# Performance work log

Measured on AMD Instinct MI355X. Metric: run time of the kernel, lower is better.

The kernel has to match this reference:

```python
import jax, jax.numpy as jnp
import numpy as np

DIM = 1024
NUM_HEADS = 16
HEAD_DIM = DIM // NUM_HEADS  # 64; only used for the softmax scale


def setup_inputs() -> dict:
    key = jax.random.key(0)
    ks = jax.random.split(key, 9)
    s = 1.0 / np.sqrt(DIM)
    return {
        "x": jax.random.normal(ks[0], (2, 4096, DIM), dtype=jnp.float32),
        "Wq": jax.random.normal(ks[1], (DIM, DIM), dtype=jnp.float32) * s,
        "bq": jnp.zeros((DIM,), dtype=jnp.float32),
        "Wk": jax.random.normal(ks[2], (DIM, DIM), dtype=jnp.float32) * s,
        "bk": jnp.zeros((DIM,), dtype=jnp.float32),
        "Wv": jax.random.normal(ks[3], (DIM, DIM), dtype=jnp.float32) * s,
        "bv": jnp.zeros((DIM,), dtype=jnp.float32),
        "Wo": jax.random.normal(ks[4], (DIM, DIM), dtype=jnp.float32) * s,
        "bo": jnp.zeros((DIM,), dtype=jnp.float32),
    }


def reference(x, Wq, bq, Wk, bk, Wv, bv, Wo, bo):
    # Projections (nn.Linear equivalents)
    q = jnp.einsum("bsd,df->bsf", x, Wq) + bq
    k = jnp.einsum("bsd,df->bsf", x, Wk) + bk
    v = jnp.einsum("bsd,df->bsf", x, Wv) + bv
    # Full-dim attention (no head split); scale uses head_dim per original code.
    scale = 1.0 / np.sqrt(HEAD_DIM)
    scores = jnp.einsum("bqd,bkd->bqk", q, k) * scale  # [B, S, S]
    attn = jax.nn.softmax(scores, axis=-1)
    out = jnp.einsum("bqk,bkd->bqd", attn, v)
    return jnp.einsum("bsd,df->bsf", out, Wo) + bo
```

## Files before the change

### kernel.cpp

```cpp
#include <hip/hip_runtime.h>

typedef unsigned short u16;
using bf16x8  = __attribute__((ext_vector_type(8))) __bf16;
using floatx4 = __attribute__((ext_vector_type(4))) float;

__device__ __forceinline__ u16 f2bf(float f) {
  unsigned int u = __builtin_bit_cast(unsigned int, f);
  u += 0x7fffu + ((u >> 16) & 1u);
  return (u16)(u >> 16);
}
__device__ __forceinline__ float bf2f(u16 h) {
  unsigned int u = ((unsigned int)h) << 16;
  return __builtin_bit_cast(float, u);
}

#define AS1(p) ((const __attribute__((address_space(1))) void*)(p))
#define AS3(p) ((__attribute__((address_space(3))) void*)(p))

#define GEMM_PROLOGUE_AT(bmv, bnv)                                           \
  __shared__ u16 As[128 * 32];                                               \
  __shared__ u16 Bs[128 * 32];                                               \
  const int tid  = threadIdx.x;                                              \
  const int wave = tid >> 6, lane = tid & 63;                                \
  const int wm = (wave >> 1) * 64, wn = (wave & 1) * 64;                     \
  const long bm = (bmv), bn = (bnv);                                         \
  floatx4 acc[4][4] = {};                                                    \
  const int srow = lane >> 2;                                                \
  const int scol = (lane & 3) * 8;                                           \
  const int c0 = wave * 2, c1 = c0 + 1;                                      \
  const int fr = lane & 15;                                                  \
  const int kq = (lane >> 4) * 8;                                            \
  const int oc = (lane >> 4) * 4;

#define GEMM_PROLOGUE() GEMM_PROLOGUE_AT((long)blockIdx.y * 128, (long)blockIdx.x * 128)

#define GEMM_STAGE(Ab, Bb, K, k0)                                            \
    __syncthreads();                                                         \
    __builtin_amdgcn_global_load_lds(AS1(Ab + (long)(c0*16 + srow)*K + k0 + scol), AS3(As + c0*512), 16, 0, 0); \
    __builtin_amdgcn_global_load_lds(AS1(Ab + (long)(c1*16 + srow)*K + k0 + scol), AS3(As + c1*512), 16, 0, 0); \
    __builtin_amdgcn_global_load_lds(AS1(Bb + (long)(c0*16 + srow)*K + k0 + scol), AS3(Bs + c0*512), 16, 0, 0); \
    __builtin_amdgcn_global_load_lds(AS1(Bb + (long)(c1*16 + srow)*K + k0 + scol), AS3(Bs + c1*512), 16, 0, 0); \
    __syncthreads();                                                         \
    bf16x8 af[4], bfv[4];                                                    \
    _Pragma("unroll")                                                        \
    for (int mi = 0; mi < 4; ++mi)                                           \
      af[mi] = *(const bf16x8*)(As + (wm + mi*16 + fr)*32 + kq);             \
    _Pragma("unroll")                                                        \
    for (int ni = 0; ni < 4; ++ni)                                           \
      bfv[ni] = *(const bf16x8*)(Bs + (wn + ni*16 + fr)*32 + kq);

#define GEMM_KSTEP_SWAP(Ab, Bb, K, k0)                                       \
  {                                                                          \
    GEMM_STAGE(Ab, Bb, K, k0)                                                \
    _Pragma("unroll")                                                        \
    for (int mi = 0; mi < 4; ++mi)                                           \
      _Pragma("unroll")                                                      \
      for (int ni = 0; ni < 4; ++ni)                                         \
        acc[mi][ni] = __builtin_amdgcn_mfma_f32_16x16x32_bf16(bfv[ni], af[mi], acc[mi][ni], 0, 0, 0); \
  }

#define NE_PROLOGUE(bmv, bnv)                                                \
  __shared__ u16 lds[65536];                                    \
  const int tid = threadIdx.x;                                               \
  const int w = tid >> 6, lane = tid & 63;                                   \
  const int wm = (w >> 2) * 128, wn = (w & 3) * 64;                          \
  const int wm16 = (w >> 2) * 8;           \
  const int wn4  = (w & 3) * 4;            \
  const long bm = (bmv), bn = (bnv);                                         \
  floatx4 acc[8][4] = {};                                                    \
  const int fr = lane & 15;                                                  \
  const int kq = (lane >> 4) * 8;                                            \
  const int oc = (lane >> 4) * 4;                                            \
         \
  const int swz  = (lane * 16) ^ (((lane >> 5) & 1) << 5);                   \
  const int srow = swz >> 6;                  \
  const int scol = (swz & 63) >> 1;           \
  const int st0  = w * 2;                      \
                        \
  const int aoff = fr * 64 + ((kq * 2) ^ (((fr >> 3) & 1) << 5));

#define NE_SETUP_PTRS(Abp, Bbp, ldK)                                         \
  const u16* A0p = (Abp) + (long)(st0 * 16 + srow) * (ldK) + scol;           \
  const u16* A1p = A0p + 16L * (ldK);                                        \
  const u16* B0p = (Bbp) + (long)(st0 * 16 + srow) * (ldK) + scol;           \
  const u16* B1p = B0p + 16L * (ldK);

#define NE_SA(T)                                                             \
  { u16* d_ = lds + (((T) & 3) * 16384) + st0 * 512;                         \
    long o_ = (long)(T) * 32;                                                \
    __builtin_amdgcn_global_load_lds(AS1(A0p + o_), AS3(d_), 16, 0, 0);      \
    __builtin_amdgcn_global_load_lds(AS1(A1p + o_), AS3(d_ + 512), 16, 0, 0); }
#define NE_SB(T)                                                             \
  { u16* d_ = lds + (((T) & 3) * 16384) + 8192 + st0 * 512;                  \
    long o_ = (long)(T) * 32;                                                \
    __builtin_amdgcn_global_load_lds(AS1(B0p + o_), AS3(d_), 16, 0, 0);      \
    __builtin_amdgcn_global_load_lds(AS1(B1p + o_), AS3(d_ + 512), 16, 0, 0); }

#define NE_TILE_G(T, NT, MF)                                                 \
  {                                                                          \
    const char* sb_ = (const char*)lds + ((T) & 3) * 32768;                  \
    if ((T) + 2 < (NT)) NE_SB((T) + 2)                                       \
    if ((T) + 3 < (NT)) NE_SA((T) + 3)                                       \
    bf16x8 af[4], bf[4];                                                     \
    _Pragma("unroll")                                                        \
    for (int i = 0; i < 4; ++i)                                              \
      af[i] = *(const bf16x8*)(sb_ + (wm16 + i) * 1024 + aoff);              \
    _Pragma("unroll")                                                        \
    for (int i = 0; i < 4; ++i)                                              \
      bf[i] = *(const bf16x8*)(sb_ + 16384 + (wn4 + i) * 1024 + aoff);       \
    asm volatile("s_waitcnt lgkmcnt(0)" ::: "memory");                       \
    __builtin_amdgcn_sched_barrier(0);                                       \
    __builtin_amdgcn_s_setprio(1);                                           \
    _Pragma("unroll")                                                        \
    for (int mi = 0; mi < 4; ++mi)                                           \
      _Pragma("unroll")                                                      \
      for (int ni = 0; ni < 4; ++ni)                                         \
        acc[mi][ni] = MF(mi, ni, acc[mi][ni]);                               \
    __builtin_amdgcn_s_setprio(0);                                           \
    _Pragma("unroll")                                                        \
    for (int i = 0; i < 4; ++i)                                              \
      af[i] = *(const bf16x8*)(sb_ + (wm16 + 4 + i) * 1024 + aoff);          \
    asm volatile("s_waitcnt lgkmcnt(0)" ::: "memory");                       \
    __builtin_amdgcn_sched_barrier(0);                                       \
    __builtin_amdgcn_s_setprio(1);                                           \
    _Pragma("unroll")                                                        \
    for (int mi = 0; mi < 4; ++mi)                                           \
      _Pragma("unroll")                                                      \
      for (int ni = 0; ni < 4; ++ni)                                         \
        acc[4 + mi][ni] = MF(mi, ni, acc[4 + mi][ni]);                       \
    __builtin_amdgcn_s_setprio(0);                                           \
    if ((T) < (NT) - 3)       { asm volatile("s_waitcnt vmcnt(6)" ::: "memory"); } \
    else if ((T) == (NT) - 3) { asm volatile("s_waitcnt vmcnt(4)" ::: "memory"); } \
    else if ((T) == (NT) - 2) { asm volatile("s_waitcnt vmcnt(0)" ::: "memory"); } \
    __builtin_amdgcn_s_barrier();                                            \
    __builtin_amdgcn_sched_barrier(0);                                       \
  }

#define NE_MF_SWAP(mi, ni, c) __builtin_amdgcn_mfma_f32_16x16x32_bf16(bf[ni], af[mi], (c), 0, 0, 0)
#define NE_MF_NS(mi, ni, c)   __builtin_amdgcn_mfma_f32_16x16x32_bf16(af[mi], bf[ni], (c), 0, 0, 0)
#define NE_TILE(T, NT)    NE_TILE_G(T, NT, NE_MF_SWAP)
#define NE_TILE_NS(T, NT) NE_TILE_G(T, NT, NE_MF_NS)

#define NE_START()                                                           \
  NE_SA(0) NE_SB(0) NE_SA(1) NE_SB(1) NE_SA(2)                               \
  asm volatile("s_waitcnt vmcnt(6)" ::: "memory");                           \
  __builtin_amdgcn_s_barrier();                                              \
  __builtin_amdgcn_sched_barrier(0);

__global__ __launch_bounds__(256) void gemm_bt(
    const u16* __restrict__ A, const u16* __restrict__ Bt,
    float* __restrict__ Cout, const float* __restrict__ bias, int N, int K)
{
  GEMM_PROLOGUE();
  const u16* Ab = A + bm * K;
  const u16* Bb = Bt + bn * K;
  for (int k0 = 0; k0 < K; k0 += 32) GEMM_KSTEP_SWAP(Ab, Bb, K, k0);

#pragma unroll
  for (int mi = 0; mi < 4; ++mi) {
    long row = bm + wm + mi*16 + fr;
#pragma unroll
    for (int ni = 0; ni < 4; ++ni) {
      long colb = bn + wn + ni*16 + oc;
      float4 bv4 = *(const float4*)(bias + colb);
      float4 o;
      o.x = acc[mi][ni][0] + bv4.x;
      o.y = acc[mi][ni][1] + bv4.y;
      o.z = acc[mi][ni][2] + bv4.z;
      o.w = acc[mi][ni][3] + bv4.w;
      *(float4*)(Cout + row * N + colb) = o;
    }
  }
}

__global__ __launch_bounds__(512, 2) void gemm_qk_exp(
    const u16* __restrict__ q, const u16* __restrict__ k,
    u16* __restrict__ probs, float* __restrict__ lpartT, float alpha)
{
  const int N = 4096;
  const int xcd = blockIdx.x;
  const int j = blockIdx.y;
  const long b = xcd >> 2;
  const int by = (xcd & 3) * 4 + (j & 3);
  const int bx = j >> 2;

  NE_PROLOGUE((long)by * 256, (long)bx * 256);
  const u16* Ab = q + b * 4096 * 1024 + bm * 1024;
  const u16* Bb = k + b * 4096 * 1024 + bn * 1024;
  NE_SETUP_PTRS(Ab, Bb, 1024);
  u16* P = probs + b * 4096L * 4096;
  float* lp = lpartT + b * 4096 * 64;

  NE_START()
  for (int T = 0; T < 32; ++T) NE_TILE(T, 32)

  const float a2 = alpha * 1.44269504f;
  const int cg = bx * 4 + (w & 3);
#pragma unroll
  for (int mi = 0; mi < 8; ++mi) {
    long row = bm + wm + mi * 16 + fr;
    float rs = 0.f;
#pragma unroll
    for (int ni = 0; ni < 4; ++ni) {
      long colb = bn + wn + ni * 16 + oc;
      float e0 = __builtin_amdgcn_exp2f(acc[mi][ni][0] * a2);
      float e1 = __builtin_amdgcn_exp2f(acc[mi][ni][1] * a2);
      float e2 = __builtin_amdgcn_exp2f(acc[mi][ni][2] * a2);
      float e3 = __builtin_amdgcn_exp2f(acc[mi][ni][3] * a2);
      rs += (e0 + e1) + (e2 + e3);
      ushort4 o;
      o.x = f2bf(e0); o.y = f2bf(e1); o.z = f2bf(e2); o.w = f2bf(e3);
      *(ushort4*)(P + row * N + colb) = o;
    }
    rs += __shfl_xor(rs, 16);
    rs += __shfl_xor(rs, 32);
    if (lane < 16)
      lp[(bm + wm + mi * 16 + lane) * 64 + cg] = rs;
  }
}

__global__ __launch_bounds__(512, 2) void gemm_pv_splitk2(
    const u16* __restrict__ probs, const u16* __restrict__ vT,
    u16* __restrict__ pA, u16* __restrict__ pB)
{
  const int xcd = blockIdx.x;
  const int j = blockIdx.y;
  const long b = xcd >> 2;
  const int sp = (xcd >> 1) & 1;
  const int by = (xcd & 1) * 8 + (j & 7);
  const int bx = j >> 3;

  NE_PROLOGUE((long)by * 256, (long)bx * 256);
  const u16* Ab = probs + b * 4096L * 4096 + bm * 4096 + sp * 2048;
  const u16* Bb = vT + b * 1024L * 4096 + bn * 4096 + sp * 2048;
  NE_SETUP_PTRS(Ab, Bb, 4096);
  u16* part = (b ? pB : pA) + (long)sp * 4096 * 1024;

  NE_START()
  for (int T = 0; T < 64; ++T) NE_TILE(T, 64)

#pragma unroll
  for (int mi = 0; mi < 8; ++mi) {
    long row = bm + wm + mi * 16 + fr;
#pragma unroll
    for (int ni = 0; ni < 4; ++ni) {
      long colb = bn + wn + ni * 16 + oc;
      ushort4 o;
      o.x = f2bf(acc[mi][ni][0]);
      o.y = f2bf(acc[mi][ni][1]);
      o.z = f2bf(acc[mi][ni][2]);
      o.w = f2bf(acc[mi][ni][3]);
      *(ushort4*)(part + row * 1024 + colb) = o;
    }
  }
}

__global__ __launch_bounds__(512, 2) void gemm_qkv(
    const u16* __restrict__ A, const u16* __restrict__ Bt,
    u16* __restrict__ qb, u16* __restrict__ kb, u16* __restrict__ vT,
    const float* __restrict__ bq, const float* __restrict__ bk,
    const float* __restrict__ bv)
{
  const int xcd = blockIdx.x;
  const int j = blockIdx.y;
  const int by = xcd * 4 + (j & 3);
  const int bx = j >> 2;

  NE_PROLOGUE((long)by * 256, (long)bx * 256);
  const u16* Ab = A + bm * 1024;
  const u16* Bb = Bt + bn * 1024;
  NE_SETUP_PTRS(Ab, Bb, 1024);

  if (bn < 2048) {
    NE_START()
    for (int T = 0; T < 32; ++T) NE_TILE(T, 32)
    u16* C = (bn < 1024) ? qb : kb;
    const float* bias = (bn < 1024) ? bq : bk;
#pragma unroll
    for (int mi = 0; mi < 8; ++mi) {
      long row = bm + wm + mi * 16 + fr;
#pragma unroll
      for (int ni = 0; ni < 4; ++ni) {
        long colg = bn + wn + ni * 16 + oc;
        long cc = colg & 1023;
        float4 bv4 = *(const float4*)(bias + cc);
        ushort4 o;
        o.x = f2bf(acc[mi][ni][0] + bv4.x);
        o.y = f2bf(acc[mi][ni][1] + bv4.y);
        o.z = f2bf(acc[mi][ni][2] + bv4.z);
        o.w = f2bf(acc[mi][ni][3] + bv4.w);
        *(ushort4*)(C + row * 1024 + cc) = o;
      }
    }
  } else {
    NE_START()
    for (int T = 0; T < 32; ++T) NE_TILE_NS(T, 32)
    const int orow = (lane >> 4) * 4;
    const long b_ = bm >> 12;
    const long s0 = (bm & 4095) + wm;
    u16* vb = vT + b_ * (1024L * 4096);
#pragma unroll
    for (int ni = 0; ni < 4; ++ni) {
      long d = bn + wn + ni * 16 + fr - 2048;
      float bvv = bv[d];
#pragma unroll
      for (int mi = 0; mi < 8; ++mi) {
        long s = s0 + mi * 16 + orow;
        ushort4 o;
        o.x = f2bf(acc[mi][ni][0] + bvv);
        o.y = f2bf(acc[mi][ni][1] + bvv);
        o.z = f2bf(acc[mi][ni][2] + bvv);
        o.w = f2bf(acc[mi][ni][3] + bvv);
        *(ushort4*)(vb + d * 4096L + s) = o;
      }
    }
  }
}

__global__ __launch_bounds__(256) void reduce2_div_row(
    const u16* __restrict__ pA, const u16* __restrict__ pB,
    const float* __restrict__ lpartT, u16* __restrict__ ob)
{
  const int row = blockIdx.x;
  const long b = blockIdx.y;
  const int tid = threadIdx.x;
  const u16* part = b ? pB : pA;
  const float* lp = lpartT + b * 4096 * 64;
  __shared__ float sl;
  if (tid < 64) {
    float s = lp[(long)row * 64 + tid];
#pragma unroll
    for (int off = 32; off; off >>= 1) s += __shfl_down(s, off);
    if (tid == 0) sl = s;
  }
  __syncthreads();
  const float inv = 1.0f / sl;
  const long base = (long)row * 1024 + tid * 4;
  float acc4[4] = {0.f, 0.f, 0.f, 0.f};
#pragma unroll
  for (int s = 0; s < 2; ++s) {
    ushort4 p = *(const ushort4*)(part + (long)s * 4096 * 1024 + base);
    acc4[0] += bf2f(p.x); acc4[1] += bf2f(p.y);
    acc4[2] += bf2f(p.z); acc4[3] += bf2f(p.w);
  }
  ushort4 o;
  o.x = f2bf(acc4[0] * inv);
  o.y = f2bf(acc4[1] * inv);
  o.z = f2bf(acc4[2] * inv);
  o.w = f2bf(acc4[3] * inv);
  *(ushort4*)(ob + b * 4096L * 1024 + base) = o;
}

__global__ __launch_bounds__(256) void prep(
    const float* __restrict__ x, u16* __restrict__ xb,
    const float* __restrict__ W0, const float* __restrict__ W1,
    const float* __restrict__ W2, const float* __restrict__ W3,
    u16* __restrict__ O0, u16* __restrict__ O1,
    u16* __restrict__ O2, u16* __restrict__ O3)
{
  __shared__ float tile[32][33];
  int blk = blockIdx.x;
  if (blk < 8192) {
    int i = blk * 256 + threadIdx.x;
    float4 f = ((const float4*)x)[i];
    ushort4 o;
    o.x = f2bf(f.x); o.y = f2bf(f.y); o.z = f2bf(f.z); o.w = f2bf(f.w);
    ((ushort4*)xb)[i] = o;
  } else {
    blk -= 8192;
    const int z = blk >> 10, t = blk & 1023;
    const float* in = (z == 0) ? W0 : (z == 1) ? W1 : (z == 2) ? W2 : W3;
    u16* outp = (z == 0) ? O0 : (z == 1) ? O1 : (z == 2) ? O2 : O3;
    const int bx = (t & 31) * 32, by = (t >> 5) * 32;
    const int tx = threadIdx.x & 31, ty = threadIdx.x >> 5;
    for (int i = ty; i < 32; i += 8)
      tile[i][tx] = in[(long)(by + i) * 1024 + bx + tx];
    __syncthreads();
    for (int i = ty; i < 32; i += 8)
      outp[(long)(bx + i) * 1024 + by + tx] = f2bf(tile[tx][i]);
  }
}

extern "C" void kernel_launch(void* const* d_in, const int* in_sizes, int n_in,
                              void* d_out, int out_size, void* d_ws, size_t ws_size,
                              hipStream_t stream) {
  const float* x  = (const float*)d_in[0];
  const float* Wq = (const float*)d_in[1];
  const float* bq = (const float*)d_in[2];
  const float* Wk = (const float*)d_in[3];
  const float* bk = (const float*)d_in[4];
  const float* Wv = (const float*)d_in[5];
  const float* bv = (const float*)d_in[6];
  const float* Wo = (const float*)d_in[7];
  const float* bo = (const float*)d_in[8];
  float* out = (float*)d_out;

  const int B = 2, S = 4096, D = 1024;
  const long MS = (long)B * S;
  const long MB = 1L << 20;

  char* w = (char*)d_ws;
  u16* qb  = (u16*)(w);
  u16* kb  = (u16*)(w + 16 * MB);
  u16* vT  = (u16*)(w + 32 * MB);
  u16* xb  = (u16*)(w + 48 * MB);
  u16* ob  = xb;
  u16* WqkvT = (u16*)(w + 64 * MB);
  u16* WoT = WqkvT + 3072L * 1024;
  u16* probs = (u16*)(w + 72 * MB);
  u16* partA = (u16*)(w);
  u16* partB = (u16*)(w + 136 * MB);
  float* lpartT = (float*)d_out;

  prep<<<dim3(8192 + 4096), 256, 0, stream>>>(
      x, xb, Wq, Wk, Wv, Wo,
      WqkvT, WqkvT + 1024L * 1024, WqkvT + 2048L * 1024, WoT);

  gemm_qkv<<<dim3(8, 48), 512, 0, stream>>>(
      xb, WqkvT, qb, kb, vT, bq, bk, bv);

  const float scale = 0.125f;
  gemm_qk_exp<<<dim3(8, 64), 512, 0, stream>>>(
      qb, kb, probs, lpartT, scale);
  gemm_pv_splitk2<<<dim3(8, 32), 512, 0, stream>>>(
      probs, vT, partA, partB);
  reduce2_div_row<<<dim3(S, B), 256, 0, stream>>>(partA, partB, lpartT, ob);

  gemm_bt<<<dim3(D / 128, MS / 128), 256, 0, stream>>>(ob, WoT, out, bo, D, D);
}
```

Measured before the change: 369.0 us.

## Use pipelined 128x256 LDS-staged GEMM tiles for QKV and output projections

Adds a new 128x256 tile GEMM variant with a 4-stage swizzled LDS ring, direct global-to-LDS loads and counted waits. The QKV projection moves from 256x256 to 128x256 tiles with twice as many blocks. The output projection replaces the simple synchronous 128x128 kernel with the same pipelined path, aiming to hide load latency and remove per-step full barriers. Smaller tiles raise occupancy and block count but reduce operand reuse per block.

```diff
diff --git a/kernel.cpp b/kernel.cpp
--- a/kernel.cpp
+++ b/kernel.cpp
@@ -16,48 +16,6 @@
 
 #define AS1(p) ((const __attribute__((address_space(1))) void*)(p))
 #define AS3(p) ((__attribute__((address_space(3))) void*)(p))
-
-#define GEMM_PROLOGUE_AT(bmv, bnv)                                           \
-  __shared__ u16 As[128 * 32];                                               \
-  __shared__ u16 Bs[128 * 32];                                               \
-  const int tid  = threadIdx.x;                                              \
-  const int wave = tid >> 6, lane = tid & 63;                                \
-  const int wm = (wave >> 1) * 64, wn = (wave & 1) * 64;                     \
-  const long bm = (bmv), bn = (bnv);                                         \
-  floatx4 acc[4][4] = {};                                                    \
-  const int srow = lane >> 2;                                                \
-  const int scol = (lane & 3) * 8;                                           \
-  const int c0 = wave * 2, c1 = c0 + 1;                                      \
-  const int fr = lane & 15;                                                  \
-  const int kq = (lane >> 4) * 8;                                            \
-  const int oc = (lane >> 4) * 4;
-
-#define GEMM_PROLOGUE() GEMM_PROLOGUE_AT((long)blockIdx.y * 128, (long)blockIdx.x * 128)
-
-#define GEMM_STAGE(Ab, Bb, K, k0)                                            \
-    __syncthreads();                                                         \
-    __builtin_amdgcn_global_load_lds(AS1(Ab + (long)(c0*16 + srow)*K + k0 + scol), AS3(As + c0*512), 16, 0, 0); \
-    __builtin_amdgcn_global_load_lds(AS1(Ab + (long)(c1*16 + srow)*K + k0 + scol), AS3(As + c1*512), 16, 0, 0); \
-    __builtin_amdgcn_global_load_lds(AS1(Bb + (long)(c0*16 + srow)*K + k0 + scol), AS3(Bs + c0*512), 16, 0, 0); \
-    __builtin_amdgcn_global_load_lds(AS1(Bb + (long)(c1*16 + srow)*K + k0 + scol), AS3(Bs + c1*512), 16, 0, 0); \
-    __syncthreads();                                                         \
-    bf16x8 af[4], bfv[4];                                                    \
-    _Pragma("unroll")                                                        \
-    for (int mi = 0; mi < 4; ++mi)                                           \
-      af[mi] = *(const bf16x8*)(As + (wm + mi*16 + fr)*32 + kq);             \
-    _Pragma("unroll")                                                        \
-    for (int ni = 0; ni < 4; ++ni)                                           \
-      bfv[ni] = *(const bf16x8*)(Bs + (wn + ni*16 + fr)*32 + kq);
-
-#define GEMM_KSTEP_SWAP(Ab, Bb, K, k0)                                       \
-  {                                                                          \
-    GEMM_STAGE(Ab, Bb, K, k0)                                                \
-    _Pragma("unroll")                                                        \
-    for (int mi = 0; mi < 4; ++mi)                                           \
-      _Pragma("unroll")                                                      \
-      for (int ni = 0; ni < 4; ++ni)                                         \
-        acc[mi][ni] = __builtin_amdgcn_mfma_f32_16x16x32_bf16(bfv[ni], af[mi], acc[mi][ni], 0, 0, 0); \
-  }
 
 #define NE_PROLOGUE(bmv, bnv)                                                \
   __shared__ u16 lds[65536];                                    \
@@ -147,31 +105,74 @@
   __builtin_amdgcn_s_barrier();                                              \
   __builtin_amdgcn_sched_barrier(0);
 
-__global__ __launch_bounds__(256) void gemm_bt(
-    const u16* __restrict__ A, const u16* __restrict__ Bt,
-    float* __restrict__ Cout, const float* __restrict__ bias, int N, int K)
-{
-  GEMM_PROLOGUE();
-  const u16* Ab = A + bm * K;
-  const u16* Bb = Bt + bn * K;
-  for (int k0 = 0; k0 < K; k0 += 32) GEMM_KSTEP_SWAP(Ab, Bb, K, k0);
-
-#pragma unroll
-  for (int mi = 0; mi < 4; ++mi) {
-    long row = bm + wm + mi*16 + fr;
-#pragma unroll
-    for (int ni = 0; ni < 4; ++ni) {
-      long colb = bn + wn + ni*16 + oc;
-      float4 bv4 = *(const float4*)(bias + colb);
-      float4 o;
-      o.x = acc[mi][ni][0] + bv4.x;
-      o.y = acc[mi][ni][1] + bv4.y;
-      o.z = acc[mi][ni][2] + bv4.z;
-      o.w = acc[mi][ni][3] + bv4.w;
-      *(float4*)(Cout + row * N + colb) = o;
-    }
-  }
-}
+#define NE2_PROLOGUE(bmv, bnv)                                               \
+  __shared__ u16 lds[49152];                                     \
+  const int tid = threadIdx.x;                                               \
+  const int w = tid >> 6, lane = tid & 63;                                   \
+  const int wm = (w >> 2) * 64, wn = (w & 3) * 64;                           \
+  const int wm4 = (w >> 2) * 4;            \
+  const int wn4 = (w & 3) * 4;             \
+  const long bm = (bmv), bn = (bnv);                                         \
+  floatx4 acc[4][4] = {};                                                    \
+  const int fr = lane & 15;                                                  \
+  const int kq = (lane >> 4) * 8;                                            \
+  const int oc = (lane >> 4) * 4;                                            \
+  const int swz  = (lane * 16) ^ (((lane >> 5) & 1) << 5);                   \
+  const int srow = swz >> 6;                                                 \
+  const int scol = (swz & 63) >> 1;                                          \
+  const int st0  = w * 2;                                                    \
+  const int aoff = fr * 64 + ((kq * 2) ^ (((fr >> 3) & 1) << 5));
+
+#define NE2_SETUP_PTRS(Abp, Bbp, ldK)                                        \
+  const u16* A0p = (Abp) + (long)(w * 16 + srow) * (ldK) + scol;             \
+  const u16* B0p = (Bbp) + (long)(st0 * 16 + srow) * (ldK) + scol;           \
+  const u16* B1p = B0p + 16L * (ldK);
+
+#define NE2_SA(T)                                                            \
+  { u16* d_ = lds + (((T) & 3) * 12288) + w * 512;                           \
+    __builtin_amdgcn_global_load_lds(AS1(A0p + (long)(T) * 32), AS3(d_), 16, 0, 0); }
+#define NE2_SB(T)                                                            \
+  { u16* d_ = lds + (((T) & 3) * 12288) + 4096 + st0 * 512;                  \
+    long o_ = (long)(T) * 32;                                                \
+    __builtin_amdgcn_global_load_lds(AS1(B0p + o_), AS3(d_), 16, 0, 0);      \
+    __builtin_amdgcn_global_load_lds(AS1(B1p + o_), AS3(d_ + 512), 16, 0, 0); }
+
+#define NE2_TILE_G(T, NT, MF)                                                \
+  {                                                                          \
+    const char* sb_ = (const char*)lds + ((T) & 3) * 24576;                  \
+    if ((T) + 2 < (NT)) NE2_SB((T) + 2)                                      \
+    if ((T) + 3 < (NT)) NE2_SA((T) + 3)                                      \
+    bf16x8 af[4], bf[4];                                                     \
+    _Pragma("unroll")                                                        \
+    for (int i = 0; i < 4; ++i)                                              \
+      af[i] = *(const bf16x8*)(sb_ + (wm4 + i) * 1024 + aoff);               \
+    _Pragma("unroll")                                                        \
+    for (int i = 0; i < 4; ++i)                                              \
+      bf[i] = *(const bf16x8*)(sb_ + 8192 + (wn4 + i) * 1024 + aoff);        \
+    asm volatile("s_waitcnt lgkmcnt(0)" ::: "memory");                       \
+    __builtin_amdgcn_sched_barrier(0);                                       \
+    __builtin_amdgcn_s_setprio(1);                                           \
+    _Pragma("unroll")                                                        \
+    for (int mi = 0; mi < 4; ++mi)                                           \
+      _Pragma("unroll")                                                      \
+      for (int ni = 0; ni < 4; ++ni)                                         \
+        acc[mi][ni] = MF(mi, ni, acc[mi][ni]);                               \
+    __builtin_amdgcn_s_setprio(0);                                           \
+    if ((T) < (NT) - 3)       { asm volatile("s_waitcnt vmcnt(4)" ::: "memory"); } \
+    else if ((T) == (NT) - 3) { asm volatile("s_waitcnt vmcnt(3)" ::: "memory"); } \
+    else if ((T) == (NT) - 2) { asm volatile("s_waitcnt vmcnt(0)" ::: "memory"); } \
+    __builtin_amdgcn_s_barrier();                                            \
+    __builtin_amdgcn_sched_barrier(0);                                       \
+  }
+
+#define NE2_TILE(T, NT)    NE2_TILE_G(T, NT, NE_MF_SWAP)
+#define NE2_TILE_NS(T, NT) NE2_TILE_G(T, NT, NE_MF_NS)
+
+#define NE2_START()                                                          \
+  NE2_SA(0) NE2_SB(0) NE2_SA(1) NE2_SB(1) NE2_SA(2)                          \
+  asm volatile("s_waitcnt vmcnt(4)" ::: "memory");                           \
+  __builtin_amdgcn_s_barrier();                                              \
+  __builtin_amdgcn_sched_barrier(0);
 
 __global__ __launch_bounds__(512, 2) void gemm_qk_exp(
     const u16* __restrict__ q, const u16* __restrict__ k,
@@ -263,21 +264,21 @@
 {
   const int xcd = blockIdx.x;
   const int j = blockIdx.y;
-  const int by = xcd * 4 + (j & 3);
-  const int bx = j >> 2;
-
-  NE_PROLOGUE((long)by * 256, (long)bx * 256);
+  const int by = xcd * 8 + (j & 7);
+  const int bx = j >> 3;
+
+  NE2_PROLOGUE((long)by * 128, (long)bx * 256);
   const u16* Ab = A + bm * 1024;
   const u16* Bb = Bt + bn * 1024;
-  NE_SETUP_PTRS(Ab, Bb, 1024);
+  NE2_SETUP_PTRS(Ab, Bb, 1024);
 
   if (bn < 2048) {
-    NE_START()
-    for (int T = 0; T < 32; ++T) NE_TILE(T, 32)
+    NE2_START()
+    for (int T = 0; T < 32; ++T) NE2_TILE(T, 32)
     u16* C = (bn < 1024) ? qb : kb;
     const float* bias = (bn < 1024) ? bq : bk;
 #pragma unroll
-    for (int mi = 0; mi < 8; ++mi) {
+    for (int mi = 0; mi < 4; ++mi) {
       long row = bm + wm + mi * 16 + fr;
 #pragma unroll
       for (int ni = 0; ni < 4; ++ni) {
@@ -293,8 +294,8 @@
       }
     }
   } else {
-    NE_START()
-    for (int T = 0; T < 32; ++T) NE_TILE_NS(T, 32)
+    NE2_START()
+    for (int T = 0; T < 32; ++T) NE2_TILE_NS(T, 32)
     const int orow = (lane >> 4) * 4;
     const long b_ = bm >> 12;
     const long s0 = (bm & 4095) + wm;
@@ -304,7 +305,7 @@
       long d = bn + wn + ni * 16 + fr - 2048;
       float bvv = bv[d];
 #pragma unroll
-      for (int mi = 0; mi < 8; ++mi) {
+      for (int mi = 0; mi < 4; ++mi) {
         long s = s0 + mi * 16 + orow;
         ushort4 o;
         o.x = f2bf(acc[mi][ni][0] + bvv);
@@ -313,6 +314,40 @@
         o.w = f2bf(acc[mi][ni][3] + bvv);
         *(ushort4*)(vb + d * 4096L + s) = o;
       }
+    }
+  }
+}
+
+__global__ __launch_bounds__(512, 2) void gemm_bt(
+    const u16* __restrict__ A, const u16* __restrict__ Bt,
+    float* __restrict__ Cout, const float* __restrict__ bias)
+{
+  const int xcd = blockIdx.x;
+  const int j = blockIdx.y;
+  const int by = xcd * 8 + (j & 7);
+  const int bx = j >> 3;
+
+  NE2_PROLOGUE((long)by * 128, (long)bx * 256);
+  const u16* Ab = A + bm * 1024;
+  const u16* Bb = Bt + bn * 1024;
+  NE2_SETUP_PTRS(Ab, Bb, 1024);
+
+  NE2_START()
+  for (int T = 0; T < 32; ++T) NE2_TILE(T, 32)
+
+#pragma unroll
+  for (int mi = 0; mi < 4; ++mi) {
+    long row = bm + wm + mi * 16 + fr;
+#pragma unroll
+    for (int ni = 0; ni < 4; ++ni) {
+      long colb = bn + wn + ni * 16 + oc;
+      float4 bv4 = *(const float4*)(bias + colb);
+      float4 o;
+      o.x = acc[mi][ni][0] + bv4.x;
+      o.y = acc[mi][ni][1] + bv4.y;
+      o.z = acc[mi][ni][2] + bv4.z;
+      o.w = acc[mi][ni][3] + bv4.w;
+      *(float4*)(Cout + row * 1024 + colb) = o;
     }
   }
 }
@@ -396,7 +431,6 @@
   float* out = (float*)d_out;
 
   const int B = 2, S = 4096, D = 1024;
-  const long MS = (long)B * S;
   const long MB = 1L << 20;
 
   char* w = (char*)d_ws;
@@ -416,7 +450,7 @@
       x, xb, Wq, Wk, Wv, Wo,
       WqkvT, WqkvT + 1024L * 1024, WqkvT + 2048L * 1024, WoT);
 
-  gemm_qkv<<<dim3(8, 48), 512, 0, stream>>>(
+  gemm_qkv<<<dim3(8, 96), 512, 0, stream>>>(
       xb, WqkvT, qb, kb, vT, bq, bk, bv);
 
   const float scale = 0.125f;
@@ -426,5 +460,5 @@
       probs, vT, partA, partB);
   reduce2_div_row<<<dim3(S, B), 256, 0, stream>>>(partA, partB, lpartT, ob);
 
-  gemm_bt<<<dim3(D / 128, MS / 128), 256, 0, stream>>>(ob, WoT, out, bo, D, D);
-}
+  gemm_bt<<<dim3(8, 32), 512, 0, stream>>>(ob, WoT, out, bo);
+}
```

Result: no change. 372.6 us (+1.0%).
